# Performance work log

Measured on AMD Instinct MI355X. Metric: run time of the kernel, lower is better.

## Reference

```python
import jax, jax.numpy as jnp
import numpy as np

NUM_LEVELS = 16
LEVEL_DIM = 2
BASE_RES = 16
MAX_RES = 2048
HASHMAP_SIZE = 1 << 19
N_POINTS = 2000000

# Instant-NGP geometric progression of grid resolutions
_scale = np.exp2(np.log2(MAX_RES / BASE_RES) / (NUM_LEVELS - 1))
RESOLUTIONS = [int(np.ceil(BASE_RES * _scale ** l)) for l in range(NUM_LEVELS)]

# corner offsets of the unit cube, shape [8, 3]
_OFFS = np.stack(np.meshgrid([0, 1], [0, 1], [0, 1], indexing='ij'), -1).reshape(8, 3)
_PRIMES = np.array([1, 2654435761, 805459861], dtype=np.uint32)


def grid_encode(x, table):
    """x: [N,3] in [0,1]; table: [L, T, F] -> [N, L*F]."""
    offs = jnp.asarray(_OFFS, dtype=jnp.int32)          # [8,3]
    feats = []
    for l, res in enumerate(RESOLUTIONS):
        pos = x * (res - 1)                              # [N,3]
        pos_i = jnp.clip(jnp.floor(pos).astype(jnp.int32), 0, res - 2)
        frac = pos - pos_i.astype(pos.dtype)             # [N,3]
        corners = pos_i[:, None, :] + offs[None]         # [N,8,3]
        if res ** 3 <= HASHMAP_SIZE:
            # dense (collision-free) indexing for coarse levels
            idx = corners[..., 0] + res * (corners[..., 1] + res * corners[..., 2])
        else:
            # spatial hash: xor of coordinate * prime, mod table size
            c = corners.astype(jnp.uint32)
            h = (c[..., 0] * _PRIMES[0]) ^ (c[..., 1] * _PRIMES[1]) ^ (c[..., 2] * _PRIMES[2])
            idx = (h % jnp.uint32(HASHMAP_SIZE)).astype(jnp.int32)
        vals = table[l][idx]                             # [N,8,F] gather
        # multilinear interpolation weights per corner
        w = jnp.prod(jnp.where(offs[None].astype(bool), frac[:, None, :], 1.0 - frac[:, None, :]), axis=-1)  # [N,8]
        feats.append(jnp.einsum('nc,ncf->nf', w, vals))
    return jnp.concatenate(feats, axis=-1)               # [N, 32]


def setup_inputs() -> dict:
    key = jax.random.key(0)
    ks = jax.random.split(key, 6)
    x = jax.random.uniform(ks[0], (N_POINTS, 3), dtype=jnp.float32)
    table = jax.random.uniform(ks[1], (NUM_LEVELS, HASHMAP_SIZE, LEVEL_DIM),
                               dtype=jnp.float32, minval=-1e-4, maxval=1e-4)
    in_dim = NUM_LEVELS * LEVEL_DIM  # 32
    W1 = jax.random.normal(ks[2], (in_dim, 64), dtype=jnp.float32) / np.sqrt(in_dim)
    W2 = jax.random.normal(ks[3], (64, 64), dtype=jnp.float32) / 8.0
    W3 = jax.random.normal(ks[4], (64, 64), dtype=jnp.float32) / 8.0
    Wo = jax.random.normal(ks[5], (64, 1), dtype=jnp.float32) / 8.0
    z = lambda n: jnp.zeros((n,), dtype=jnp.float32)
    return {"x": x, "table": table, "W1": W1, "b1": z(64), "W2": W2, "b2": z(64),
            "W3": W3, "b3": z(64), "Wo": Wo, "bo": z(1)}


def reference(x, table, W1, b1, W2, b2, W3, b3, Wo, bo):
    h = grid_encode(x, table)                 # [N,32]
    h = jax.nn.relu(h @ W1 + b1)
    h = jax.nn.relu(h @ W2 + b2)
    h = jax.nn.relu(h @ W3 + b3)
    return h @ Wo + bo                        # [N,1]
```

## Files before the change

kernel.cpp:

```cpp
#include <hip/hip_runtime.h>
#include <cmath>
#include <cstdint>


#define HASH_SZ (1u << 19)
#define HMASK   (HASH_SZ - 1u)
#define PR2 2654435761u
#define PR3 805459861u

typedef float v2f __attribute__((ext_vector_type(2)));
typedef float v4f __attribute__((ext_vector_type(4)));
typedef v4f v4fu __attribute__((aligned(8)));
typedef v2f v2fu __attribute__((aligned(8)));
typedef short bf16x8 __attribute__((ext_vector_type(8)));
typedef float f32x4 __attribute__((ext_vector_type(4)));

struct ResArr { int r[16]; };

__device__ __forceinline__ unsigned short bf16_rne(float f) {
    union { float f; unsigned u; } v; v.f = f;
    unsigned u = v.u;
    unsigned r = (u + 0x7fffu + ((u >> 16) & 1u)) >> 16;
    return (unsigned short)r;
}
__device__ __forceinline__ float bf16f(unsigned short h) {
    union { unsigned u; float f; } v; v.u = ((unsigned)h) << 16;
    return v.f;
}
__device__ __forceinline__ void split8(const float* x, bf16x8& hi, bf16x8& lo) {
    #pragma unroll
    for (int j = 0; j < 8; ++j) {
        union { float f; unsigned u; } v; v.f = x[j];
        const unsigned hu = v.u & 0xffff0000u;
        hi[j] = (short)(hu >> 16);
        union { unsigned u; float f; } hf; hf.u = hu;
        const float d = x[j] - hf.f;
        union { float f; unsigned u; } dv; dv.f = d;
        lo[j] = (short)((dv.u + 0x7fffu + ((dv.u >> 16) & 1u)) >> 16);
    }
}

__device__ __forceinline__ void gather_one(
    const v2f* __restrict__ tbl, int res, bool dense,
    float px, float py, float pz, float& A0, float& A1)
{
    const float rf = (float)(res - 1);
    const float fx = px * rf, fy = py * rf, fz = pz * rf;
    int ix = (int)floorf(fx), iy = (int)floorf(fy), iz = (int)floorf(fz);
    ix = min(max(ix, 0), res - 2);
    iy = min(max(iy, 0), res - 2);
    iz = min(max(iz, 0), res - 2);
    const float tx = fx - (float)ix, ty = fy - (float)iy, tz = fz - (float)iz;
    const float sx = 1.f - tx, sy = 1.f - ty, sz = 1.f - tz;
    float a0 = 0.f, a1 = 0.f;

    if (dense) {
        const int b0 = ix + res * (iy + res * iz);
        v4fu P[4];
        #pragma unroll
        for (int c = 0; c < 4; ++c) {
            const int dy = c >> 1, dz = c & 1;
            P[c] = *(const v4fu*)((const float*)tbl + 2 * (b0 + res * dy + res * res * dz));
        }
        #pragma unroll
        for (int c = 0; c < 4; ++c) {
            const int dy = c >> 1, dz = c & 1;
            const float wyz = (dy ? ty : sy) * (dz ? tz : sz);
            const float w0 = sx * wyz, w1 = tx * wyz;
            a0 = fmaf(w0, P[c].x, a0); a1 = fmaf(w0, P[c].y, a1);
            a0 = fmaf(w1, P[c].z, a0); a1 = fmaf(w1, P[c].w, a1);
        }
    } else {
        uint32_t i0[4], i1[4];
        v4f P[4];
        #pragma unroll
        for (int c = 0; c < 4; ++c) {
            const int dy = c >> 1, dz = c & 1;
            const uint32_t r = (uint32_t)(iy + dy) * PR2 ^ (uint32_t)(iz + dz) * PR3;
            i0[c] = ((uint32_t)ix ^ r) & HMASK;
            i1[c] = ((uint32_t)(ix + 1) ^ r) & HMASK;
            P[c] = *(const v4f*)((const float*)tbl + 2 * (i0[c] & ~1u));
        }
        const bool odd = (ix & 1);
        v2f O[4];
        if (odd) {
            #pragma unroll
            for (int c = 0; c < 4; ++c) O[c] = tbl[i1[c]];
        } else {
            #pragma unroll
            for (int c = 0; c < 4; ++c) { v2f z = {0.f, 0.f}; O[c] = z; }
        }
        #pragma unroll
        for (int c = 0; c < 4; ++c) {
            const int dy = c >> 1, dz = c & 1;
            const bool hi = (i0[c] & 1);
            v2f c0, e;
            c0.x = hi ? P[c].z : P[c].x;  c0.y = hi ? P[c].w : P[c].y;
            e.x  = hi ? P[c].x : P[c].z;  e.y  = hi ? P[c].y : P[c].w;
            const v2f c1 = odd ? O[c] : e;
            const float wyz = (dy ? ty : sy) * (dz ? tz : sz);
            const float w0 = sx * wyz, w1 = tx * wyz;
            a0 = fmaf(w0, c0.x, a0); a1 = fmaf(w0, c0.y, a1);
            a0 = fmaf(w1, c1.x, a0); a1 = fmaf(w1, c1.y, a1);
        }
    }
    A0 = a0; A1 = a1;
}

template<int NLEV>
__global__ __launch_bounds__(256, 8)
void encode_k(const float* __restrict__ x, const float* __restrict__ table,
              v2f* __restrict__ featT, int n, int lb, ResArr rv)
{
    const int nth2 = gridDim.x * 512;
    for (int q = (blockIdx.x * 256 + threadIdx.x) * 2; q < n; q += nth2) {
        float p0x, p0y, p0z, p1x, p1y, p1z;
        const bool two = (q + 1 < n);
        if (two) {
            const v4fu a = __builtin_nontemporal_load((const v4fu*)(x + 3 * q));
            const v2f  b = __builtin_nontemporal_load((const v2fu*)(x + 3 * q + 4));
            p0x = a.x; p0y = a.y; p0z = a.z; p1x = a.w; p1y = b.x; p1z = b.y;
        } else {
            p0x = x[3 * q]; p0y = x[3 * q + 1]; p0z = x[3 * q + 2];
            p1x = p0x; p1y = p0y; p1z = p0z;
        }
        #pragma unroll
        for (int il = 0; il < NLEV; ++il) {
            const int l = lb + il;
            const int res = rv.r[l];
            const bool dense = ((long long)res * res * res <= (long long)HASH_SZ);
            const v2f* tbl = (const v2f*)table + (size_t)l * HASH_SZ;
            float a00, a01, a10, a11;
            gather_one(tbl, res, dense, p0x, p0y, p0z, a00, a01);
            gather_one(tbl, res, dense, p1x, p1y, p1z, a10, a11);
            if (two) {
                v4f st; st.x = a00; st.y = a01; st.z = a10; st.w = a11;
                __builtin_nontemporal_store(st, (v4f*)&featT[(size_t)l * n + q]);
            } else {
                v2f st; st.x = a00; st.y = a01;
                __builtin_nontemporal_store(st, &featT[(size_t)l * n + q]);
            }
        }
    }
}

__global__ void prep_weights(const float* __restrict__ W1,
                             const float* __restrict__ W2,
                             const float* __restrict__ W3,
                             unsigned short* __restrict__ wb)
{
    const int tid = threadIdx.x;
    const int nb = tid >> 6, lane = tid & 63;
    const int l15 = lane & 15, q = lane >> 4;
    #pragma unroll
    for (int j = 0; j < 8; ++j) {
        const float v = W1[(q * 8 + j) * 64 + nb * 16 + l15];
        const unsigned short h = bf16_rne(v);
        wb[(nb * 64 + lane) * 8 + j] = h;
        wb[2048 + (nb * 64 + lane) * 8 + j] = bf16_rne(v - bf16f(h));
    }
    #pragma unroll
    for (int kb = 0; kb < 2; ++kb) {
        #pragma unroll
        for (int j = 0; j < 8; ++j) {
            const int row = kb * 32 + q * 8 + j;
            const int idx = ((kb * 4 + nb) * 64 + lane) * 8 + j;
            float v = W2[row * 64 + nb * 16 + l15];
            unsigned short h = bf16_rne(v);
            wb[4096 + idx] = h;
            wb[8192 + idx] = bf16_rne(v - bf16f(h));
            v = W3[row * 64 + nb * 16 + l15];
            h = bf16_rne(v);
            wb[12288 + idx] = h;
            wb[16384 + idx] = bf16_rne(v - bf16f(h));
        }
    }
}

#define TSTR 65

__global__ __launch_bounds__(256, 4)
void mlp_mfma(const v2f* __restrict__ featT,
              const unsigned short* __restrict__ wb,
              const float* __restrict__ b1, const float* __restrict__ b2,
              const float* __restrict__ b3,
              const float* __restrict__ Wo, const float* __restrict__ bo,
              float* __restrict__ out, int n)
{
    __shared__ float sact[4][32 * TSTR];
    const int wave = threadIdx.x >> 6;
    const int lane = threadIdx.x & 63;
    const int l15 = lane & 15, quad = lane >> 4;
    const int p0 = (blockIdx.x * 4 + wave) * 32;
    if (p0 >= n) return;

    bf16x8 ah[2], al[2];
    #pragma unroll
    for (int t = 0; t < 2; ++t) {
        const int p = p0 + t * 16 + l15;
        const int pl = (p < n) ? p : (n - 1);
        float xv[8];
        #pragma unroll
        for (int jj = 0; jj < 4; ++jj) {
            const v2f f = featT[(size_t)(quad * 4 + jj) * n + pl];
            xv[2 * jj] = f.x; xv[2 * jj + 1] = f.y;
        }
        split8(xv, ah[t], al[t]);
    }

    f32x4 acc[2][4];
    #pragma unroll
    for (int nb = 0; nb < 4; ++nb) {
        const bf16x8 wh = *(const bf16x8*)(wb + (nb * 64 + lane) * 8);
        const bf16x8 wl = *(const bf16x8*)(wb + 2048 + (nb * 64 + lane) * 8);
        const float bv = b1[nb * 16 + l15];
        #pragma unroll
        for (int t = 0; t < 2; ++t) {
            f32x4 c = {bv, bv, bv, bv};
            c = __builtin_amdgcn_mfma_f32_16x16x32_bf16(ah[t], wl, c, 0, 0, 0);
            c = __builtin_amdgcn_mfma_f32_16x16x32_bf16(al[t], wh, c, 0, 0, 0);
            c = __builtin_amdgcn_mfma_f32_16x16x32_bf16(ah[t], wh, c, 0, 0, 0);
            acc[t][nb] = c;
        }
    }

    #pragma unroll
    for (int layer = 0; layer < 2; ++layer) {
        #pragma unroll
        for (int t = 0; t < 2; ++t)
            #pragma unroll
            for (int nb = 0; nb < 4; ++nb)
                #pragma unroll
                for (int r = 0; r < 4; ++r)
                    sact[wave][(t * 16 + quad * 4 + r) * TSTR + nb * 16 + l15] =
                        fmaxf(acc[t][nb][r], 0.f);

        bf16x8 a2h[2][2], a2l[2][2];
        #pragma unroll
        for (int t = 0; t < 2; ++t) {
            float x2[16];
            #pragma unroll
            for (int kb = 0; kb < 2; ++kb)
                #pragma unroll
                for (int j = 0; j < 8; ++j)
                    x2[kb * 8 + j] =
                        sact[wave][(t * 16 + l15) * TSTR + kb * 32 + quad * 8 + j];
            split8(x2,     a2h[t][0], a2l[t][0]);
            split8(x2 + 8, a2h[t][1], a2l[t][1]);
        }

        const int base_h = layer ? 12288 : 4096;
        const int base_l = layer ? 16384 : 8192;
        const float* __restrict__ bias = layer ? b3 : b2;
        #pragma unroll
        for (int nb = 0; nb < 4; ++nb) {
            const float bv = bias[nb * 16 + l15];
            f32x4 c[2];
            #pragma unroll
            for (int t = 0; t < 2; ++t) { f32x4 z = {bv, bv, bv, bv}; c[t] = z; }
            #pragma unroll
            for (int kb = 0; kb < 2; ++kb) {
                const int idx = ((kb * 4 + nb) * 64 + lane) * 8;
                const bf16x8 wh = *(const bf16x8*)(wb + base_h + idx);
                const bf16x8 wl = *(const bf16x8*)(wb + base_l + idx);
                #pragma unroll
                for (int t = 0; t < 2; ++t) {
                    c[t] = __builtin_amdgcn_mfma_f32_16x16x32_bf16(a2h[t][kb], wl, c[t], 0, 0, 0);
                    c[t] = __builtin_amdgcn_mfma_f32_16x16x32_bf16(a2l[t][kb], wh, c[t], 0, 0, 0);
                    c[t] = __builtin_amdgcn_mfma_f32_16x16x32_bf16(a2h[t][kb], wh, c[t], 0, 0, 0);
                }
            }
            #pragma unroll
            for (int t = 0; t < 2; ++t) acc[t][nb] = c[t];
        }
    }

    const float wo = Wo[0 * 16 + l15];
    (void)wo;
    float part[2][4];
    #pragma unroll
    for (int t = 0; t < 2; ++t)
        #pragma unroll
        for (int r = 0; r < 4; ++r) {
            float s = 0.f;
            #pragma unroll
            for (int nb = 0; nb < 4; ++nb)
                s = fmaf(fmaxf(acc[t][nb][r], 0.f), Wo[nb * 16 + l15], s);
            part[t][r] = s;
        }
    #pragma unroll
    for (int mask = 1; mask < 16; mask <<= 1)
        #pragma unroll
        for (int t = 0; t < 2; ++t)
            #pragma unroll
            for (int r = 0; r < 4; ++r)
                part[t][r] += __shfl_xor(part[t][r], mask, 64);

    if (l15 == 0) {
        const float b = bo[0];
        #pragma unroll
        for (int t = 0; t < 2; ++t)
            #pragma unroll
            for (int r = 0; r < 4; ++r) {
                const int po = p0 + t * 16 + quad * 4 + r;
                if (po < n) out[po] = part[t][r] + b;
            }
    }
}

__global__ __launch_bounds__(256, 3)
void mlp_forward(const v2f* __restrict__ featT,
                 const float* __restrict__ W1, const float* __restrict__ b1,
                 const float* __restrict__ W2, const float* __restrict__ b2,
                 const float* __restrict__ W3, const float* __restrict__ b3,
                 const float* __restrict__ Wo, const float* __restrict__ bo,
                 float* __restrict__ out, int n)
{
    const int p = blockIdx.x * 256 + threadIdx.x;
    if (p >= n) return;
    const v2f z2 = {0.f, 0.f};
    v2f A[32], B[32];
    #pragma unroll
    for (int jq = 0; jq < 16; ++jq) {
        const v4f b = *(const v4f*)(b1 + 4 * jq);
        A[2 * jq] = b.xy; A[2 * jq + 1] = b.zw;
    }
    #pragma unroll
    for (int l = 0; l < 16; ++l) {
        const v2f f = __builtin_nontemporal_load(&featT[(size_t)l * n + p]);
        const v4f* w0 = (const v4f*)(W1 + (size_t)(2 * l) * 64);
        const v4f* w1 = (const v4f*)(W1 + (size_t)(2 * l + 1) * 64);
        const v2f h0 = {f.x, f.x}, h1 = {f.y, f.y};
        #pragma unroll
        for (int jq = 0; jq < 16; ++jq) {
            const v4f wa = w0[jq];
            A[2 * jq]     = __builtin_elementwise_fma(h0, wa.xy, A[2 * jq]);
            A[2 * jq + 1] = __builtin_elementwise_fma(h0, wa.zw, A[2 * jq + 1]);
        }
        #pragma unroll
        for (int jq = 0; jq < 16; ++jq) {
            const v4f wb2 = w1[jq];
            A[2 * jq]     = __builtin_elementwise_fma(h1, wb2.xy, A[2 * jq]);
            A[2 * jq + 1] = __builtin_elementwise_fma(h1, wb2.zw, A[2 * jq + 1]);
        }
    }
    #pragma unroll
    for (int j = 0; j < 32; ++j) A[j] = __builtin_elementwise_max(A[j], z2);
    #pragma unroll
    for (int jq = 0; jq < 16; ++jq) {
        const v4f b = *(const v4f*)(b2 + 4 * jq);
        B[2 * jq] = b.xy; B[2 * jq + 1] = b.zw;
    }
    #pragma unroll
    for (int k = 0; k < 64; ++k) {
        const float hv = A[k >> 1][k & 1];
        const v2f h = {hv, hv};
        const v4f* w = (const v4f*)(W2 + (size_t)k * 64);
        #pragma unroll
        for (int jq = 0; jq < 16; ++jq) {
            const v4f wa = w[jq];
            B[2 * jq]     = __builtin_elementwise_fma(h, wa.xy, B[2 * jq]);
            B[2 * jq + 1] = __builtin_elementwise_fma(h, wa.zw, B[2 * jq + 1]);
        }
    }
    #pragma unroll
    for (int j = 0; j < 32; ++j) B[j] = __builtin_elementwise_max(B[j], z2);
    #pragma unroll
    for (int jq = 0; jq < 16; ++jq) {
        const v4f b = *(const v4f*)(b3 + 4 * jq);
        A[2 * jq] = b.xy; A[2 * jq + 1] = b.zw;
    }
    #pragma unroll
    for (int k = 0; k < 64; ++k) {
        const float hv = B[k >> 1][k & 1];
        const v2f h = {hv, hv};
        const v4f* w = (const v4f*)(W3 + (size_t)k * 64);
        #pragma unroll
        for (int jq = 0; jq < 16; ++jq) {
            const v4f wa = w[jq];
            A[2 * jq]     = __builtin_elementwise_fma(h, wa.xy, A[2 * jq]);
            A[2 * jq + 1] = __builtin_elementwise_fma(h, wa.zw, A[2 * jq + 1]);
        }
    }
    v2f o2 = z2;
    #pragma unroll
    for (int jq = 0; jq < 16; ++jq) {
        const v4f wa = *(const v4f*)(Wo + 4 * jq);
        o2 = __builtin_elementwise_fma(__builtin_elementwise_max(A[2 * jq], z2),     wa.xy, o2);
        o2 = __builtin_elementwise_fma(__builtin_elementwise_max(A[2 * jq + 1], z2), wa.zw, o2);
    }
    out[p] = o2.x + o2.y + bo[0];
}

__global__ __launch_bounds__(256, 2)
void hashpinn_fused(const float* __restrict__ x,
                    const float* __restrict__ table,
                    const float* __restrict__ W1, const float* __restrict__ b1,
                    const float* __restrict__ W2, const float* __restrict__ b2,
                    const float* __restrict__ W3, const float* __restrict__ b3,
                    const float* __restrict__ Wo, const float* __restrict__ bo,
                    float* __restrict__ out, int n, ResArr rv)
{
    const int p = blockIdx.x * 256 + threadIdx.x;
    if (p >= n) return;
    const float px = x[3*p+0], py = x[3*p+1], pz = x[3*p+2];
    float feat[32];
    #pragma unroll
    for (int l = 0; l < 16; ++l) {
        const int res = rv.r[l];
        const float rf = (float)(res - 1);
        const float fx = px*rf, fy = py*rf, fz = pz*rf;
        int ix=(int)floorf(fx), iy=(int)floorf(fy), iz=(int)floorf(fz);
        ix=min(max(ix,0),res-2); iy=min(max(iy,0),res-2); iz=min(max(iz,0),res-2);
        const float tx=fx-(float)ix, ty=fy-(float)iy, tz=fz-(float)iz;
        const float sx=1.f-tx, sy=1.f-ty, sz=1.f-tz;
        const float2* tbl=(const float2*)table+(size_t)l*HASH_SZ;
        const bool dense=((long long)res*res*res<=(long long)HASH_SZ);
        float a0=0.f, a1=0.f;
        #pragma unroll
        for (int c=0;c<8;++c){
            const uint32_t cx=(uint32_t)(ix+((c>>2)&1));
            const uint32_t cy=(uint32_t)(iy+((c>>1)&1));
            const uint32_t cz=(uint32_t)(iz+(c&1));
            uint32_t idx = dense ? cx+(uint32_t)res*(cy+(uint32_t)res*cz)
                                 : ((cx*1u ^ cy*PR2 ^ cz*PR3)&HMASK);
            const float2 v=tbl[idx];
            const float w=(((c>>2)&1)?tx:sx)*(((c>>1)&1)?ty:sy)*((c&1)?tz:sz);
            a0=fmaf(w,v.x,a0); a1=fmaf(w,v.y,a1);
        }
        feat[2*l]=a0; feat[2*l+1]=a1;
    }
    float A[64], B[64];
    #pragma unroll
    for (int j=0;j<64;++j) A[j]=b1[j];
    #pragma unroll
    for (int k=0;k<32;++k){ const float h=feat[k];
        #pragma unroll
        for (int j=0;j<64;++j) A[j]=fmaf(h,W1[k*64+j],A[j]); }
    #pragma unroll 1
    for (int it=0;it<2;++it){
        const float* W = it?W3:W2; const float* bb = it?b3:b2;
        #pragma unroll
        for (int j=0;j<64;++j){ A[j]=fmaxf(A[j],0.f); B[j]=bb[j]; }
        #pragma unroll
        for (int k=0;k<64;++k){ const float h=A[k];
            #pragma unroll
            for (int j=0;j<64;++j) B[j]=fmaf(h,W[k*64+j],B[j]); }
        #pragma unroll
        for (int j=0;j<64;++j) A[j]=B[j];
    }
    float o=bo[0];
    #pragma unroll
    for (int j=0;j<64;++j) o=fmaf(fmaxf(A[j],0.f),Wo[j],o);
    out[p]=o;
}

static inline void launch_encode(int nlev, const float* x, const float* table,
                                 v2f* featT, int n, int lb, const ResArr& rv,
                                 hipStream_t stream) {
    const dim3 g(4096), b(256);
    switch (nlev) {
        case 1: hipLaunchKernelGGL(encode_k<1>, g, b, 0, stream, x, table, featT, n, lb, rv); break;
        case 2: hipLaunchKernelGGL(encode_k<2>, g, b, 0, stream, x, table, featT, n, lb, rv); break;
        case 3: hipLaunchKernelGGL(encode_k<3>, g, b, 0, stream, x, table, featT, n, lb, rv); break;
        case 4: hipLaunchKernelGGL(encode_k<4>, g, b, 0, stream, x, table, featT, n, lb, rv); break;
        case 5: hipLaunchKernelGGL(encode_k<5>, g, b, 0, stream, x, table, featT, n, lb, rv); break;
        case 6: hipLaunchKernelGGL(encode_k<6>, g, b, 0, stream, x, table, featT, n, lb, rv); break;
        case 7: hipLaunchKernelGGL(encode_k<7>, g, b, 0, stream, x, table, featT, n, lb, rv); break;
        default: hipLaunchKernelGGL(encode_k<8>, g, b, 0, stream, x, table, featT, n, lb, rv); break;
    }
}

extern "C" void kernel_launch(void* const* d_in, const int* in_sizes, int n_in,
                              void* d_out, int out_size, void* d_ws, size_t ws_size,
                              hipStream_t stream) {
    const float* x     = (const float*)d_in[0];
    const float* table = (const float*)d_in[1];
    const float* W1    = (const float*)d_in[2];
    const float* b1    = (const float*)d_in[3];
    const float* W2    = (const float*)d_in[4];
    const float* b2    = (const float*)d_in[5];
    const float* W3    = (const float*)d_in[6];
    const float* b3    = (const float*)d_in[7];
    const float* Wo    = (const float*)d_in[8];
    const float* bo    = (const float*)d_in[9];
    float* out = (float*)d_out;

    const int n = in_sizes[0] / 3;

    ResArr rv;
    const double scale = std::exp2(std::log2(2048.0 / 16.0) / 15.0);
    for (int l = 0; l < 16; ++l)
        rv.r[l] = (int)std::ceil(16.0 * std::pow(scale, (double)l));

    int dense_end = 0;
    while (dense_end < 16) {
        long long r = rv.r[dense_end];
        if (r * r * r <= (long long)HASH_SZ) ++dense_end; else break;
    }
    if (dense_end > 8) dense_end = 8;

    const size_t feat_bytes = (size_t)n * 16 * sizeof(v2f);
    const size_t wb_bytes = 20480 * sizeof(unsigned short);

    if (ws_size >= feat_bytes + wb_bytes) {
        v2f* featT = (v2f*)d_ws;
        unsigned short* wb = (unsigned short*)((char*)d_ws + feat_bytes);

        hipLaunchKernelGGL(prep_weights, dim3(1), dim3(256), 0, stream, W1, W2, W3, wb);

        if (dense_end > 0)
            launch_encode(dense_end, x, table, featT, n, 0, rv, stream);
        for (int l = dense_end; l < 16; ++l)
            launch_encode(1, x, table, featT, n, l, rv, stream);

        const int nblocks = (n + 127) / 128;
        hipLaunchKernelGGL(mlp_mfma, dim3(nblocks), dim3(256), 0, stream,
                           featT, wb, b1, b2, b3, Wo, bo, out, n);
    } else if (ws_size >= feat_bytes) {
        v2f* featT = (v2f*)d_ws;
        if (dense_end > 0)
            launch_encode(dense_end, x, table, featT, n, 0, rv, stream);
        for (int l = dense_end; l < 16; ++l)
            launch_encode(1, x, table, featT, n, l, rv, stream);
        hipLaunchKernelGGL(mlp_forward, dim3((n + 255) / 256), dim3(256), 0, stream,
                           featT, W1, b1, W2, b2, W3, b3, Wo, bo, out, n);
    } else {
        hipLaunchKernelGGL(hashpinn_fused, dim3((n + 255) / 256), dim3(256), 0, stream,
                           x, table, W1, b1, W2, b2, W3, b3, Wo, bo, out, n, rv);
    }
}
```

Baseline: 1.085 ms.

## Convert hashed table levels to fp16 and gather paired corners

Adds a per-call pass that converts the hashed-level embedding table to packed fp16, then a new encode kernel gathers from this half-size table. Because the hash uses xor with ix, the x-neighbour corners usually sit in the same aligned pair, so one 8-byte load often fetches both. The MLP kernel also gets an XOR-swizzled shared-memory layout with vector reads and a higher occupancy launch bound. The cost is an extra conversion pass over the table every call and fp16 rounding of the table values.

```diff
diff --git a/kernel.cpp b/kernel.cpp
--- a/kernel.cpp
+++ b/kernel.cpp
@@ -14,6 +14,8 @@
 typedef v2f v2fu __attribute__((aligned(8)));
 typedef short bf16x8 __attribute__((ext_vector_type(8)));
 typedef float f32x4 __attribute__((ext_vector_type(4)));
+typedef unsigned u2 __attribute__((ext_vector_type(2)));
+typedef _Float16 f16x2 __attribute__((ext_vector_type(2)));
 
 struct ResArr { int r[16]; };
 
@@ -38,6 +40,10 @@
         union { float f; unsigned u; } dv; dv.f = d;
         lo[j] = (short)((dv.u + 0x7fffu + ((dv.u >> 16) & 1u)) >> 16);
     }
+}
+__device__ __forceinline__ v2f h2f(unsigned u) {
+    union { unsigned u; f16x2 h; } c; c.u = u;
+    v2f r; r.x = (float)c.h.x; r.y = (float)c.h.y; return r;
 }
 
 __device__ __forceinline__ void gather_one(
@@ -144,6 +150,96 @@
     }
 }
 
+__global__ void prep_table16(const float* __restrict__ table,
+                             unsigned* __restrict__ tbl16,
+                             int base_entries, int total)
+{
+    const int i = blockIdx.x * 256 + threadIdx.x;
+    if (i >= total) return;
+    const v2f v = *(const v2f*)(table + 2 * (size_t)(base_entries + i));
+    f16x2 h; h.x = (_Float16)v.x; h.y = (_Float16)v.y;
+    union { f16x2 h; unsigned u; } cv; cv.h = h;
+    tbl16[i] = cv.u;
+}
+
+__device__ __forceinline__ void gather_hash16(
+    const unsigned* __restrict__ tbl, int res,
+    float px, float py, float pz, float& A0, float& A1)
+{
+    const float rf = (float)(res - 1);
+    const float fx = px * rf, fy = py * rf, fz = pz * rf;
+    int ix = (int)floorf(fx), iy = (int)floorf(fy), iz = (int)floorf(fz);
+    ix = min(max(ix, 0), res - 2);
+    iy = min(max(iy, 0), res - 2);
+    iz = min(max(iz, 0), res - 2);
+    const float tx = fx - (float)ix, ty = fy - (float)iy, tz = fz - (float)iz;
+    const float sx = 1.f - tx, sy = 1.f - ty, sz = 1.f - tz;
+
+    uint32_t i0[4], i1[4];
+    u2 pr[4];
+    #pragma unroll
+    for (int c = 0; c < 4; ++c) {
+        const int dy = c >> 1, dz = c & 1;
+        const uint32_t r = (uint32_t)(iy + dy) * PR2 ^ (uint32_t)(iz + dz) * PR3;
+        i0[c] = ((uint32_t)ix ^ r) & HMASK;
+        i1[c] = ((uint32_t)(ix + 1) ^ r) & HMASK;
+        pr[c] = *(const u2*)(tbl + (i0[c] & ~1u));
+    }
+    const bool odd = (ix & 1);
+    unsigned sg[4];
+    if (odd) {
+        #pragma unroll
+        for (int c = 0; c < 4; ++c) sg[c] = tbl[i1[c]];
+    } else {
+        #pragma unroll
+        for (int c = 0; c < 4; ++c) sg[c] = 0u;
+    }
+    float a0 = 0.f, a1 = 0.f;
+    #pragma unroll
+    for (int c = 0; c < 4; ++c) {
+        const int dy = c >> 1, dz = c & 1;
+        const bool hi = (i0[c] & 1);
+        const unsigned c0u = hi ? pr[c].y : pr[c].x;
+        const unsigned eu  = hi ? pr[c].x : pr[c].y;
+        const unsigned c1u = odd ? sg[c] : eu;
+        const v2f c0 = h2f(c0u), c1 = h2f(c1u);
+        const float wyz = (dy ? ty : sy) * (dz ? tz : sz);
+        const float w0 = sx * wyz, w1 = tx * wyz;
+        a0 = fmaf(w0, c0.x, a0); a1 = fmaf(w0, c0.y, a1);
+        a0 = fmaf(w1, c1.x, a0); a1 = fmaf(w1, c1.y, a1);
+    }
+    A0 = a0; A1 = a1;
+}
+
+__global__ __launch_bounds__(256, 8)
+void encode_hash16(const float* __restrict__ x, const unsigned* __restrict__ tbl,
+                   v2f* __restrict__ featT, int n, int l, int res)
+{
+    const int nth2 = gridDim.x * 512;
+    for (int q = (blockIdx.x * 256 + threadIdx.x) * 2; q < n; q += nth2) {
+        float p0x, p0y, p0z, p1x, p1y, p1z;
+        const bool two = (q + 1 < n);
+        if (two) {
+            const v4fu a = __builtin_nontemporal_load((const v4fu*)(x + 3 * q));
+            const v2f  b = __builtin_nontemporal_load((const v2fu*)(x + 3 * q + 4));
+            p0x = a.x; p0y = a.y; p0z = a.z; p1x = a.w; p1y = b.x; p1z = b.y;
+        } else {
+            p0x = x[3 * q]; p0y = x[3 * q + 1]; p0z = x[3 * q + 2];
+            p1x = p0x; p1y = p0y; p1z = p0z;
+        }
+        float a00, a01, a10, a11;
+        gather_hash16(tbl, res, p0x, p0y, p0z, a00, a01);
+        gather_hash16(tbl, res, p1x, p1y, p1z, a10, a11);
+        if (two) {
+            v4f st; st.x = a00; st.y = a01; st.z = a10; st.w = a11;
+            __builtin_nontemporal_store(st, (v4f*)&featT[(size_t)l * n + q]);
+        } else {
+            v2f st; st.x = a00; st.y = a01;
+            __builtin_nontemporal_store(st, &featT[(size_t)l * n + q]);
+        }
+    }
+}
+
 __global__ void prep_weights(const float* __restrict__ W1,
                              const float* __restrict__ W2,
                              const float* __restrict__ W3,
@@ -177,9 +273,7 @@
     }
 }
 
-#define TSTR 65
-
-__global__ __launch_bounds__(256, 4)
+__global__ __launch_bounds__(256, 5)
 void mlp_mfma(const v2f* __restrict__ featT,
               const unsigned short* __restrict__ wb,
               const float* __restrict__ b1, const float* __restrict__ b2,
@@ -187,11 +281,11 @@
               const float* __restrict__ Wo, const float* __restrict__ bo,
               float* __restrict__ out, int n)
 {
-    __shared__ float sact[4][32 * TSTR];
-    const int wave = threadIdx.x >> 6;
+    __shared__ float sact[4 * 32 * 64];
+    float* __restrict__ sw = sact + (threadIdx.x >> 6) * (32 * 64);
     const int lane = threadIdx.x & 63;
     const int l15 = lane & 15, quad = lane >> 4;
-    const int p0 = (blockIdx.x * 4 + wave) * 32;
+    const int p0 = (blockIdx.x * 4 + (threadIdx.x >> 6)) * 32;
     if (p0 >= n) return;
 
     bf16x8 ah[2], al[2];
@@ -231,20 +325,27 @@
             #pragma unroll
             for (int nb = 0; nb < 4; ++nb)
                 #pragma unroll
-                for (int r = 0; r < 4; ++r)
-                    sact[wave][(t * 16 + quad * 4 + r) * TSTR + nb * 16 + l15] =
-                        fmaxf(acc[t][nb][r], 0.f);
+                for (int r = 0; r < 4; ++r) {
+                    const int row = t * 16 + quad * 4 + r;
+                    const int col = nb * 16 + l15;
+                    const int idx = row * 64 + ((((col >> 2) ^ (row & 15)) << 2) | (col & 3));
+                    sw[idx] = fmaxf(acc[t][nb][r], 0.f);
+                }
 
         bf16x8 a2h[2][2], a2l[2][2];
         #pragma unroll
         for (int t = 0; t < 2; ++t) {
+            const int row = t * 16 + l15;
             float x2[16];
             #pragma unroll
             for (int kb = 0; kb < 2; ++kb)
                 #pragma unroll
-                for (int j = 0; j < 8; ++j)
-                    x2[kb * 8 + j] =
-                        sact[wave][(t * 16 + l15) * TSTR + kb * 32 + quad * 8 + j];
+                for (int cp = 0; cp < 2; ++cp) {
+                    const int chunk = kb * 8 + quad * 2 + cp;
+                    const v4f v = *(const v4f*)&sw[row * 64 + ((chunk ^ (row & 15)) << 2)];
+                    #pragma unroll
+                    for (int w = 0; w < 4; ++w) x2[kb * 8 + cp * 4 + w] = v[w];
+                }
             split8(x2,     a2h[t][0], a2l[t][0]);
             split8(x2 + 8, a2h[t][1], a2l[t][1]);
         }
@@ -275,8 +376,6 @@
         }
     }
 
-    const float wo = Wo[0 * 16 + l15];
-    (void)wo;
     float part[2][4];
     #pragma unroll
     for (int t = 0; t < 2; ++t)
@@ -501,21 +600,37 @@
     if (dense_end > 8) dense_end = 8;
 
     const size_t feat_bytes = (size_t)n * 16 * sizeof(v2f);
-    const size_t wb_bytes = 20480 * sizeof(unsigned short);
-
-    if (ws_size >= feat_bytes + wb_bytes) {
+    const size_t wb_bytes   = 20480 * sizeof(unsigned short);
+    const int    h_entries  = (16 - dense_end) * (int)HASH_SZ;
+    const size_t t16_bytes  = (size_t)h_entries * sizeof(unsigned);
+
+    if (ws_size >= feat_bytes + wb_bytes + t16_bytes) {
         v2f* featT = (v2f*)d_ws;
         unsigned short* wb = (unsigned short*)((char*)d_ws + feat_bytes);
+        unsigned* tbl16 = (unsigned*)((char*)d_ws + feat_bytes + wb_bytes);
 
         hipLaunchKernelGGL(prep_weights, dim3(1), dim3(256), 0, stream, W1, W2, W3, wb);
-
+        hipLaunchKernelGGL(prep_table16, dim3((h_entries + 255) / 256), dim3(256), 0, stream,
+                           table, tbl16, dense_end * (int)HASH_SZ, h_entries);
+
+        if (dense_end > 0)
+            launch_encode(dense_end, x, table, featT, n, 0, rv, stream);
+        for (int l = dense_end; l < 16; ++l)
+            hipLaunchKernelGGL(encode_hash16, dim3(4096), dim3(256), 0, stream,
+                               x, tbl16 + (size_t)(l - dense_end) * HASH_SZ,
+                               featT, n, l, rv.r[l]);
+
+        hipLaunchKernelGGL(mlp_mfma, dim3((n + 127) / 128), dim3(256), 0, stream,
+                           featT, wb, b1, b2, b3, Wo, bo, out, n);
+    } else if (ws_size >= feat_bytes + wb_bytes) {
+        v2f* featT = (v2f*)d_ws;
+        unsigned short* wb = (unsigned short*)((char*)d_ws + feat_bytes);
+        hipLaunchKernelGGL(prep_weights, dim3(1), dim3(256), 0, stream, W1, W2, W3, wb);
         if (dense_end > 0)
             launch_encode(dense_end, x, table, featT, n, 0, rv, stream);
         for (int l = dense_end; l < 16; ++l)
             launch_encode(1, x, table, featT, n, l, rv, stream);
-
-        const int nblocks = (n + 127) / 128;
-        hipLaunchKernelGGL(mlp_mfma, dim3(nblocks), dim3(256), 0, stream,
+        hipLaunchKernelGGL(mlp_mfma, dim3((n + 127) / 128), dim3(256), 0, stream,
                            featT, wb, b1, b2, b3, Wo, bo, out, n);
     } else if (ws_size >= feat_bytes) {
         v2f* featT = (v2f*)d_ws;
```

Measured after the change: 1.223 ms. 12.7% more time.
